# Optimization experiments

Measured on AMD Instinct MI355X. Metric: run time of the kernel, lower is better.

Reference implementation:

```python
import jax, jax.numpy as jnp
import numpy as np

NUM_LETTERS = 33
EMB = 64
HID = 512
KPT = 21
CRD = 3
SEQ = 100
IN0 = EMB * 2 + KPT * CRD * 2  # 254


def setup_inputs() -> dict:
    key = jax.random.key(0)
    ks = jax.random.split(key, 16)
    B = 4096
    s = 0.05
    return {
        "start_letters": jax.random.randint(ks[0], (B,), 0, NUM_LETTERS, dtype=jnp.int32),
        "end_letters": jax.random.randint(ks[1], (B,), 0, NUM_LETTERS, dtype=jnp.int32),
        "start_coords": jax.random.normal(ks[2], (B, KPT * CRD), jnp.float32),
        "end_coords": jax.random.normal(ks[3], (B, KPT * CRD), jnp.float32),
        "emb": jax.random.normal(ks[4], (NUM_LETTERS, EMB), jnp.float32) * s,
        "W_ih0": jax.random.normal(ks[5], (4 * HID, IN0), jnp.float32) * s,
        "W_hh0": jax.random.normal(ks[6], (4 * HID, HID), jnp.float32) * s,
        "b_ih0": jax.random.normal(ks[7], (4 * HID,), jnp.float32) * s,
        "b_hh0": jax.random.normal(ks[8], (4 * HID,), jnp.float32) * s,
        "W_ih1": jax.random.normal(ks[9], (4 * HID, HID), jnp.float32) * s,
        "W_hh1": jax.random.normal(ks[10], (4 * HID, HID), jnp.float32) * s,
        "b_ih1": jax.random.normal(ks[11], (4 * HID,), jnp.float32) * s,
        "b_hh1": jax.random.normal(ks[12], (4 * HID,), jnp.float32) * s,
        "fc_W": jax.random.normal(ks[13], (KPT * CRD, HID), jnp.float32) * s,
        "fc_b": jax.random.normal(ks[14], (KPT * CRD,), jnp.float32) * s,
    }


def _lstm_cell(pre, c):
    # PyTorch gate order: input, forget, cell(g), output
    i, f, g, o = jnp.split(pre, 4, axis=-1)
    c_new = jax.nn.sigmoid(f) * c + jax.nn.sigmoid(i) * jnp.tanh(g)
    h_new = jax.nn.sigmoid(o) * jnp.tanh(c_new)
    return h_new, c_new


def reference(start_letters, end_letters, start_coords, end_coords,
              emb, W_ih0, W_hh0, b_ih0, b_hh0, W_ih1, W_hh1, b_ih1, b_hh1,
              fc_W, fc_b):
    # combined input, constant across timesteps: [B, 254]
    x = jnp.concatenate([emb[start_letters], emb[end_letters],
                         start_coords, end_coords], axis=-1)
    B = x.shape[0]
    # layer-0 input projection is constant per step -> hoist out of the scan
    x0 = x @ W_ih0.T + b_ih0 + b_hh0  # [B, 4H]
    b1 = b_ih1 + b_hh1

    def step(carry, _):
        h0, c0, h1, c1 = carry
        h0, c0 = _lstm_cell(x0 + h0 @ W_hh0.T, c0)
        h1, c1 = _lstm_cell(h0 @ W_ih1.T + b1 + h1 @ W_hh1.T, c1)
        y = h1 @ fc_W.T + fc_b  # [B, 63]
        return (h0, c0, h1, c1), y

    z = jnp.zeros((B, HID), x.dtype)
    _, ys = jax.lax.scan(step, (z, z, z, z), None, length=SEQ)  # [T, B, 63]
    # -> [B, keypoints, coords, T]
    return jnp.moveaxis(ys, 0, -1).reshape(B, KPT, CRD, SEQ)
```

## Files before the change

### kernel.cpp

```cpp
#include <hip/hip_runtime.h>


#define HIDN  512
#define SEQL  100
#define BATCH 4096
#define NB    8
#define BR    128

typedef _Float16 f16;
typedef _Float16 half8 __attribute__((ext_vector_type(8)));
typedef float    f32x4 __attribute__((ext_vector_type(4)));
typedef unsigned int u32x4 __attribute__((ext_vector_type(4)));

#define OFF_XCAT   0ul
#define OFF_X0PT   (OFF_XCAT + 256ul*4096*4)
#define OFF_WP0    (OFF_X0PT + 2048ul*4096*4)
#define OFF_WP1I   (OFF_WP0  + 2048ul*512*2)
#define OFF_WP1H   (OFF_WP1I + 2048ul*512*2)
#define OFF_FCW    (OFF_WP1H + 2048ul*512*2)
#define OFF_B1P    (OFF_FCW  + 64ul*512*2)
#define OFF_H0     (OFF_B1P  + 2048ul*4)
#define OFF_H1     (OFF_H0   + 2ul*4096*512*2)
#define OFF_FLAGS  (OFF_H1   + 2ul*4096*512*2)
#define FLAG_BYTES (32ul*128*4)

__device__ __forceinline__ int orow(int pr){
  return (((pr>>6)&3)<<9) | ((pr>>8)<<6) | (pr&63);
}
__device__ __forceinline__ float sigm(float x){ return 1.f/(1.f + __expf(-x)); }
__device__ __forceinline__ float tanhx(float x){ return 1.f - 2.f/(1.f + __expf(2.f*x)); }
__device__ __forceinline__ f32x4 splat4(float v){ f32x4 r; r[0]=v; r[1]=v; r[2]=v; r[3]=v; return r; }

__global__ __launch_bounds__(256) void k_xcat(
    const int* __restrict__ sl, const int* __restrict__ el,
    const float* __restrict__ sc, const float* __restrict__ ec,
    const float* __restrict__ emb, float* __restrict__ xcatT)
{
  int b = blockIdx.x*256 + threadIdx.x;
  int c = blockIdx.y;
  float v = 0.f;
  if      (c < 64 ) v = emb[sl[b]*64 + c];
  else if (c < 128) v = emb[el[b]*64 + (c-64)];
  else if (c < 191) v = sc[b*63 + (c-128)];
  else if (c < 254) v = ec[b*63 + (c-191)];
  xcatT[c*4096 + b] = v;
}

__global__ __launch_bounds__(256) void k_pack(
    const float* __restrict__ Whh0, const float* __restrict__ Wih1,
    const float* __restrict__ Whh1, const float* __restrict__ fcW,
    const float* __restrict__ bih1, const float* __restrict__ bhh1,
    f16* __restrict__ Wp0, f16* __restrict__ Wp1i, f16* __restrict__ Wp1h,
    f16* __restrict__ fcWp, float* __restrict__ b1p)
{
  int row = blockIdx.x, tid = threadIdx.x;
  if (row < 6144){
    int m  = row >> 11;
    int pr = row & 2047;
    const float* src = (m==0) ? Whh0 : (m==1) ? Wih1 : Whh1;
    f16* dst = (m==0) ? Wp0 : (m==1) ? Wp1i : Wp1h;
    int orig = orow(pr);
    dst[pr*512 + tid      ] = (f16)src[orig*512 + tid      ];
    dst[pr*512 + tid + 256] = (f16)src[orig*512 + tid + 256];
  } else if (row < 6208){
    int n = row - 6144;
    float v0 = (n < 63) ? fcW[n*512 + tid      ] : 0.f;
    float v1 = (n < 63) ? fcW[n*512 + tid + 256] : 0.f;
    fcWp[n*512 + tid] = (f16)v0; fcWp[n*512 + tid + 256] = (f16)v1;
  } else {
    int j = row - 6208;
    int orig = (((tid>>6)&3)<<9) | (j<<6) | (tid&63);
    b1p[j*256 + tid] = bih1[orig] + bhh1[orig];
  }
}

__global__ __launch_bounds__(256) void k_x0(
    const float* __restrict__ xcatT, const float* __restrict__ Wih0,
    const float* __restrict__ bih0, const float* __restrict__ bhh0,
    float* __restrict__ x0pT)
{
  int pr0 = blockIdx.x * 16;
  int b   = blockIdx.y * 256 + threadIdx.x;
  float a[16];
#pragma unroll
  for (int i=0;i<16;i++) a[i] = 0.f;
  for (int k=0;k<254;k++){
    float xv = xcatT[k*4096 + b];
#pragma unroll
    for (int i=0;i<16;i++)
      a[i] = fmaf(xv, Wih0[orow(pr0+i)*254 + k], a[i]);
  }
#pragma unroll
  for (int i=0;i<16;i++){
    int orig = orow(pr0+i);
    x0pT[(size_t)(pr0+i)*4096 + b] = a[i] + bih0[orig] + bhh0[orig];
  }
}

__global__ __launch_bounds__(512, 2) void k_lstm(
    const float* __restrict__ x0pT, const f16* __restrict__ Wp0,
    const f16* __restrict__ Wp1i, const f16* __restrict__ Wp1h,
    const f16* __restrict__ fcWp, const float* __restrict__ b1p,
    const float* __restrict__ fcb, f16* __restrict__ h0buf,
    f16* __restrict__ h1buf, unsigned int* __restrict__ flags,
    float* __restrict__ out)
{
  __shared__ f16 Ach[2][128*40];
  __shared__ f16 Bch[2][256*40];

  const int tid  = threadIdx.x;
  const int blk  = blockIdx.x;
  const int j    = blk & 7;
  const int team = blk >> 3;
  const int b0   = team * BR;
  const int w = tid >> 6, wr = w >> 2, wc = w & 3;
  const int lane = tid & 63, quad = lane >> 4, lc = lane & 15;
  const int ucol = wc*16 + lc;
  const bool des = (j == (team & 7));

  const f16* Wb0  = Wp0  + (size_t)(j*256)*512;
  const f16* Wb1i = Wp1i + (size_t)(j*256)*512;
  const f16* Wb1h = Wp1h + (size_t)(j*256)*512;

  float b1v[4];
#pragma unroll
  for (int g=0; g<4; g++) b1v[g] = b1p[j*256 + g*64 + ucol];
  const float fcbv = (ucol < 63) ? fcb[ucol] : 0.f;

  f32x4 c0[4], c1[4];
#pragma unroll
  for (int mt=0; mt<4; mt++){ c0[mt] = splat4(0.f); c1[mt] = splat4(0.f); }

  const int srA = tid >> 2;
  const int ssg = (tid & 3) * 8;
  unsigned int* tflags = flags + team*128;

  auto barrier = [&](int idx){
    __syncthreads();
    if (tid == 0){
      __threadfence();
      __hip_atomic_fetch_add(&tflags[idx], 1u, __ATOMIC_RELAXED, __HIP_MEMORY_SCOPE_AGENT);
      while (__hip_atomic_load(&tflags[idx], __ATOMIC_RELAXED, __HIP_MEMORY_SCOPE_AGENT) < (unsigned)NB)
        __builtin_amdgcn_s_sleep(4);
      __threadfence();
    }
    __syncthreads();
  };

  auto GEMM = [&](int nch, auto&& Aat, auto&& Bat, f32x4 (&acc)[4][4],
                  bool dofc, f32x4* fca, int fck0){
    u32x4 ra, rb0, rb1;
    auto ld = [&](int kc){
      const f16* Ap = Aat(kc);
      const f16* Bp = Bat(kc);
      ra  = *(const u32x4*)(Ap + (size_t)srA*HIDN + ssg);
      rb0 = *(const u32x4*)(Bp + (size_t)srA*HIDN + ssg);
      rb1 = *(const u32x4*)(Bp + (size_t)(srA+128)*HIDN + ssg);
    };
    auto st = [&](int kc){
      int bu = kc & 1;
      *(u32x4*)&Ach[bu][srA*40 + ssg]        = ra;
      *(u32x4*)&Bch[bu][srA*40 + ssg]        = rb0;
      *(u32x4*)&Bch[bu][(srA+128)*40 + ssg]  = rb1;
    };
    ld(0); st(0);
    if (nch > 1) ld(1);
    for (int kc=0; kc<nch; kc++){
      __syncthreads();
      if (kc+1 < nch){
        st(kc+1);
        if (kc+2 < nch) ld(kc+2);
      }
      const int bu = kc & 1;
      half8 af[4];
#pragma unroll
      for (int mt=0; mt<4; mt++)
        af[mt] = *(const half8*)&Ach[bu][(wr*64 + mt*16 + lc)*40 + quad*8];
#pragma unroll
      for (int g=0; g<4; g++){
        half8 bf = *(const half8*)&Bch[bu][(g*64 + ucol)*40 + quad*8];
#pragma unroll
        for (int mt=0; mt<4; mt++)
          acc[g][mt] = __builtin_amdgcn_mfma_f32_16x16x32_f16(af[mt], bf, acc[g][mt], 0, 0, 0);
      }
      if (dofc && kc >= fck0){
        half8 fb = *(const half8*)(fcWp + (size_t)ucol*HIDN + (kc-fck0)*32 + quad*8);
#pragma unroll
        for (int mt=0; mt<4; mt++)
          fca[mt] = __builtin_amdgcn_mfma_f32_16x16x32_f16(af[mt], fb, fca[mt], 0, 0, 0);
      }
    }
  };

  for (int t=0; t<SEQL; t++){
    const int p  = t & 1;
    const int pp = (t-1) & 1;
    const f16* h0rd = h0buf + (size_t)pp*BATCH*HIDN + (size_t)b0*HIDN;
    const f16* h1rd = h1buf + (size_t)pp*BATCH*HIDN + (size_t)b0*HIDN;
    f16* h0wr = h0buf + (size_t)p*BATCH*HIDN;
    f16* h1wr = h1buf + (size_t)p*BATCH*HIDN;

    f32x4 acc[4][4];
#pragma unroll
    for (int g=0; g<4; g++)
#pragma unroll
      for (int mt=0; mt<4; mt++)
        acc[g][mt] = *(const f32x4*)(x0pT + (size_t)(j*256 + g*64 + ucol)*4096
                                     + b0 + wr*64 + mt*16 + quad*4);
    if (t > 0){
      GEMM(16, [&](int kc){ return h0rd + kc*32; },
               [&](int kc){ return Wb0  + kc*32; },
           acc, false, (f32x4*)nullptr, 0);
    }
#pragma unroll
    for (int mt=0; mt<4; mt++){
#pragma unroll
      for (int r=0; r<4; r++){
        float iv = sigm(acc[0][mt][r]);
        float fv = sigm(acc[1][mt][r]);
        float gv = tanhx(acc[2][mt][r]);
        float ov = sigm(acc[3][mt][r]);
        float cn = fv*c0[mt][r] + iv*gv;
        c0[mt][r] = cn;
        float hn = ov * tanhx(cn);
        int row = wr*64 + mt*16 + quad*4 + r;
        h0wr[(size_t)(b0+row)*HIDN + j*64 + ucol] = (f16)hn;
      }
    }
    barrier(t);

    const f16* h0cur = h0buf + (size_t)p*BATCH*HIDN + (size_t)b0*HIDN;
#pragma unroll
    for (int g=0; g<4; g++)
#pragma unroll
      for (int mt=0; mt<4; mt++)
        acc[g][mt] = splat4(b1v[g]);
    f32x4 fca[4];
#pragma unroll
    for (int mt=0; mt<4; mt++) fca[mt] = splat4(fcbv);

    if (t > 0){
      GEMM(32, [&](int kc){ return kc < 16 ? h0cur + kc*32 : h1rd  + (kc-16)*32; },
               [&](int kc){ return kc < 16 ? Wb1i  + kc*32 : Wb1h + (kc-16)*32; },
           acc, des, fca, 16);
      if (des && ucol < 63){
#pragma unroll
        for (int mt=0; mt<4; mt++)
#pragma unroll
          for (int r=0; r<4; r++){
            int row = wr*64 + mt*16 + quad*4 + r;
            out[((b0+row)*63 + ucol)*100 + (t-1)] = fca[mt][r];
          }
      }
    } else {
      GEMM(16, [&](int kc){ return h0cur + kc*32; },
               [&](int kc){ return Wb1i  + kc*32; },
           acc, false, (f32x4*)nullptr, 0);
    }
#pragma unroll
    for (int mt=0; mt<4; mt++){
#pragma unroll
      for (int r=0; r<4; r++){
        float iv = sigm(acc[0][mt][r]);
        float fv = sigm(acc[1][mt][r]);
        float gv = tanhx(acc[2][mt][r]);
        float ov = sigm(acc[3][mt][r]);
        float cn = fv*c1[mt][r] + iv*gv;
        c1[mt][r] = cn;
        float hn = ov * tanhx(cn);
        int row = wr*64 + mt*16 + quad*4 + r;
        h1wr[(size_t)(b0+row)*HIDN + j*64 + ucol] = (f16)hn;
      }
    }
  }

  barrier(SEQL);
  if (des){
    const f16* h1last = h1buf + (size_t)1*BATCH*HIDN + (size_t)b0*HIDN;
    f32x4 fca[4];
#pragma unroll
    for (int mt=0; mt<4; mt++) fca[mt] = splat4(fcbv);
    for (int kc=0; kc<16; kc++){
      __syncthreads();
      *(u32x4*)&Ach[0][srA*40 + ssg] = *(const u32x4*)(h1last + (size_t)srA*HIDN + kc*32 + ssg);
      __syncthreads();
      half8 af[4];
#pragma unroll
      for (int mt=0; mt<4; mt++)
        af[mt] = *(const half8*)&Ach[0][(wr*64 + mt*16 + lc)*40 + quad*8];
      half8 fb = *(const half8*)(fcWp + (size_t)ucol*HIDN + kc*32 + quad*8);
#pragma unroll
      for (int mt=0; mt<4; mt++)
        fca[mt] = __builtin_amdgcn_mfma_f32_16x16x32_f16(af[mt], fb, fca[mt], 0, 0, 0);
    }
    if (ucol < 63){
#pragma unroll
      for (int mt=0; mt<4; mt++)
#pragma unroll
        for (int r=0; r<4; r++){
          int row = wr*64 + mt*16 + quad*4 + r;
          out[((b0+row)*63 + ucol)*100 + 99] = fca[mt][r];
        }
    }
  }
}

extern "C" void kernel_launch(void* const* d_in, const int* in_sizes, int n_in,
                              void* d_out, int out_size, void* d_ws, size_t ws_size,
                              hipStream_t stream)
{
  const int*   sl   = (const int*)  d_in[0];
  const int*   el   = (const int*)  d_in[1];
  const float* sc   = (const float*)d_in[2];
  const float* ec   = (const float*)d_in[3];
  const float* emb  = (const float*)d_in[4];
  const float* Wih0 = (const float*)d_in[5];
  const float* Whh0 = (const float*)d_in[6];
  const float* bih0 = (const float*)d_in[7];
  const float* bhh0 = (const float*)d_in[8];
  const float* Wih1 = (const float*)d_in[9];
  const float* Whh1 = (const float*)d_in[10];
  const float* bih1 = (const float*)d_in[11];
  const float* bhh1 = (const float*)d_in[12];
  const float* fcW  = (const float*)d_in[13];
  const float* fcb  = (const float*)d_in[14];

  char* ws = (char*)d_ws;
  float* xcatT = (float*)(ws + OFF_XCAT);
  float* x0pT  = (float*)(ws + OFF_X0PT);
  f16*   Wp0   = (f16*)  (ws + OFF_WP0);
  f16*   Wp1i  = (f16*)  (ws + OFF_WP1I);
  f16*   Wp1h  = (f16*)  (ws + OFF_WP1H);
  f16*   fcWp  = (f16*)  (ws + OFF_FCW);
  float* b1p   = (float*)(ws + OFF_B1P);
  f16*   h0b   = (f16*)  (ws + OFF_H0);
  f16*   h1b   = (f16*)  (ws + OFF_H1);
  unsigned int* flags = (unsigned int*)(ws + OFF_FLAGS);

  hipMemsetAsync(flags, 0, FLAG_BYTES, stream);
  k_xcat<<<dim3(16, 256), 256, 0, stream>>>(sl, el, sc, ec, emb, xcatT);
  k_pack<<<6216, 256, 0, stream>>>(Whh0, Wih1, Whh1, fcW, bih1, bhh1,
                                   Wp0, Wp1i, Wp1h, fcWp, b1p);
  k_x0<<<dim3(128, 16), 256, 0, stream>>>(xcatT, Wih0, bih0, bhh0, x0pT);
  k_lstm<<<256, 512, 0, stream>>>(x0pT, Wp0, Wp1i, Wp1h, fcWp, b1p, fcb,
                                  h0b, h1b, flags, (float*)d_out);
}
```

Measured before the change: 8.291 ms.

## Pre-swizzle weights into MFMA fragment layout and stage larger swizzled A tiles

Weights are repacked on the device into per-lane MFMA fragment order, so each lane loads its B fragments directly from global memory with software prefetch two k-chunks ahead, and B no longer goes through LDS. The A (hidden state) tile is staged in halves of 256 columns into a single XOR-swizzled LDS buffer, which cuts the number of __syncthreads per GEMM from one per k-chunk to a few per pass. The x0 projection is also written in a fragment-friendly layout so accumulator initialisation becomes contiguous vector loads. The trade-off is more registers per thread and a larger LDS footprint (64KB), which may limit occupancy at two blocks per CU.

After: 17.84 ms. 2.15x slower.

```diff
diff --git a/kernel.cpp b/kernel.cpp
--- a/kernel.cpp
+++ b/kernel.cpp
@@ -13,12 +13,12 @@
 typedef unsigned int u32x4 __attribute__((ext_vector_type(4)));
 
 #define OFF_XCAT   0ul
-#define OFF_X0PT   (OFF_XCAT + 256ul*4096*4)
-#define OFF_WP0    (OFF_X0PT + 2048ul*4096*4)
-#define OFF_WP1I   (OFF_WP0  + 2048ul*512*2)
-#define OFF_WP1H   (OFF_WP1I + 2048ul*512*2)
-#define OFF_FCW    (OFF_WP1H + 2048ul*512*2)
-#define OFF_B1P    (OFF_FCW  + 64ul*512*2)
+#define OFF_X0F    (OFF_XCAT + 256ul*4096*4)
+#define OFF_BF0    (OFF_X0F  + 2048ul*4096*4)
+#define OFF_BF1I   (OFF_BF0  + 2048ul*512*2)
+#define OFF_BF1H   (OFF_BF1I + 2048ul*512*2)
+#define OFF_FCF    (OFF_BF1H + 2048ul*512*2)
+#define OFF_B1P    (OFF_FCF  + 64ul*512*2)
 #define OFF_H0     (OFF_B1P  + 2048ul*4)
 #define OFF_H1     (OFF_H0   + 2ul*4096*512*2)
 #define OFF_FLAGS  (OFF_H1   + 2ul*4096*512*2)
@@ -50,34 +50,55 @@
     const float* __restrict__ Whh0, const float* __restrict__ Wih1,
     const float* __restrict__ Whh1, const float* __restrict__ fcW,
     const float* __restrict__ bih1, const float* __restrict__ bhh1,
-    f16* __restrict__ Wp0, f16* __restrict__ Wp1i, f16* __restrict__ Wp1h,
-    f16* __restrict__ fcWp, float* __restrict__ b1p)
+    f16* __restrict__ BF0, f16* __restrict__ BF1i, f16* __restrict__ BF1h,
+    f16* __restrict__ fcF, float* __restrict__ b1p)
 {
-  int row = blockIdx.x, tid = threadIdx.x;
-  if (row < 6144){
-    int m  = row >> 11;
-    int pr = row & 2047;
+  int bx = blockIdx.x, t = threadIdx.x;
+  if (bx < 384){
+    int m   = bx / 128;
+    int rem = bx % 128;
+    int jj = rem >> 4, g = (rem >> 2) & 3, wc = rem & 3;
     const float* src = (m==0) ? Whh0 : (m==1) ? Wih1 : Whh1;
-    f16* dst = (m==0) ? Wp0 : (m==1) ? Wp1i : Wp1h;
-    int orig = orow(pr);
-    dst[pr*512 + tid      ] = (f16)src[orig*512 + tid      ];
-    dst[pr*512 + tid + 256] = (f16)src[orig*512 + tid + 256];
-  } else if (row < 6208){
-    int n = row - 6144;
-    float v0 = (n < 63) ? fcW[n*512 + tid      ] : 0.f;
-    float v1 = (n < 63) ? fcW[n*512 + tid + 256] : 0.f;
-    fcWp[n*512 + tid] = (f16)v0; fcWp[n*512 + tid + 256] = (f16)v1;
+    f16* dst = (m==0) ? BF0 : (m==1) ? BF1i : BF1h;
+    size_t fb = (size_t)(((jj*4+g)*4+wc)*16) * 512;
+    for (int s=0; s<4; s++){
+      int pid = t + s*256;
+      int kc = pid >> 6, lane = pid & 63;
+      int lcc = lane & 15, qd = lane >> 4;
+      int orig = g*512 + jj*64 + wc*16 + lcc;
+      const float* sp = src + (size_t)orig*512 + kc*32 + qd*8;
+      f16* d = dst + fb + (size_t)kc*512 + lane*8;
+#pragma unroll
+      for (int e=0; e<8; e++) d[e] = (f16)sp[e];
+    }
+  } else if (bx < 388){
+    int wc = bx - 384;
+    for (int s=0; s<4; s++){
+      int pid = t + s*256;
+      int kc = pid >> 6, lane = pid & 63;
+      int lcc = lane & 15, qd = lane >> 4;
+      int col = wc*16 + lcc;
+      f16* d = fcF + (size_t)(wc*16 + kc)*512 + lane*8;
+      if (col < 63){
+        const float* sp = fcW + (size_t)col*512 + kc*32 + qd*8;
+#pragma unroll
+        for (int e=0; e<8; e++) d[e] = (f16)sp[e];
+      } else {
+#pragma unroll
+        for (int e=0; e<8; e++) d[e] = (f16)0.f;
+      }
+    }
   } else {
-    int j = row - 6208;
-    int orig = (((tid>>6)&3)<<9) | (j<<6) | (tid&63);
-    b1p[j*256 + tid] = bih1[orig] + bhh1[orig];
+    int jj = bx - 388;
+    int orig = (((t>>6)&3)<<9) | (jj<<6) | (t&63);
+    b1p[jj*256 + t] = bih1[orig] + bhh1[orig];
   }
 }
 
 __global__ __launch_bounds__(256) void k_x0(
     const float* __restrict__ xcatT, const float* __restrict__ Wih0,
     const float* __restrict__ bih0, const float* __restrict__ bhh0,
-    float* __restrict__ x0pT)
+    float* __restrict__ x0F)
 {
   int pr0 = blockIdx.x * 16;
   int b   = blockIdx.y * 256 + threadIdx.x;
@@ -90,23 +111,27 @@
     for (int i=0;i<16;i++)
       a[i] = fmaf(xv, Wih0[orow(pr0+i)*254 + k], a[i]);
   }
+  int team = b>>7, wrr = (b>>6)&1, mtt = (b>>4)&3, qd = (b>>2)&3, r = b&3;
 #pragma unroll
   for (int i=0;i<16;i++){
-    int orig = orow(pr0+i);
-    x0pT[(size_t)(pr0+i)*4096 + b] = a[i] + bih0[orig] + bhh0[orig];
+    int pr = pr0 + i;
+    int orig = orow(pr);
+    int jj = pr>>8, g = (pr>>6)&3, u = pr&63, wcc = u>>4, lcc = u&15;
+    size_t idx = (size_t)team*262144 + (size_t)jj*32768 + g*8192 + wrr*4096
+               + mtt*1024 + wcc*256 + (qd*16 + lcc)*4 + r;
+    x0F[idx] = a[i] + bih0[orig] + bhh0[orig];
   }
 }
 
 __global__ __launch_bounds__(512, 2) void k_lstm(
-    const float* __restrict__ x0pT, const f16* __restrict__ Wp0,
-    const f16* __restrict__ Wp1i, const f16* __restrict__ Wp1h,
-    const f16* __restrict__ fcWp, const float* __restrict__ b1p,
+    const float* __restrict__ x0F, const f16* __restrict__ BF0,
+    const f16* __restrict__ BF1i, const f16* __restrict__ BF1h,
+    const f16* __restrict__ fcF, const float* __restrict__ b1p,
     const float* __restrict__ fcb, f16* __restrict__ h0buf,
     f16* __restrict__ h1buf, unsigned int* __restrict__ flags,
     float* __restrict__ out)
 {
-  __shared__ f16 Ach[2][128*40];
-  __shared__ f16 Bch[2][256*40];
+  __shared__ f16 Ash[128*256];
 
   const int tid  = threadIdx.x;
   const int blk  = blockIdx.x;
@@ -118,9 +143,13 @@
   const int ucol = wc*16 + lc;
   const bool des = (j == (team & 7));
 
-  const f16* Wb0  = Wp0  + (size_t)(j*256)*512;
-  const f16* Wb1i = Wp1i + (size_t)(j*256)*512;
-  const f16* Wb1h = Wp1h + (size_t)(j*256)*512;
+  const size_t fboff = (size_t)(((j*4)*4+wc)*16)*512 + lane*8;
+  const f16* Bb0  = BF0  + fboff;
+  const f16* Bb1i = BF1i + fboff;
+  const f16* Bb1h = BF1h + fboff;
+  const f16* fcp = fcF + (size_t)(wc*16)*512 + lane*8;
+  const float* x0p = x0F + (size_t)team*262144 + (size_t)j*32768
+                   + wr*4096 + wc*256 + lane*4;
 
   float b1v[4];
 #pragma unroll
@@ -131,10 +160,13 @@
 #pragma unroll
   for (int mt=0; mt<4; mt++){ c0[mt] = splat4(0.f); c1[mt] = splat4(0.f); }
 
-  const int srA = tid >> 2;
-  const int ssg = (tid & 3) * 8;
+  const int srow  = tid >> 2;
+  const int sslot = tid & 3;
+  const int swzb  = (quad*16) ^ ((lc&3)<<4);
+  const int swzf  = (lc&4)<<4;
+  char* Abase = (char*)Ash + (wr*64 + lc)*512 + swzb;
+
   unsigned int* tflags = flags + team*128;
-
   auto barrier = [&](int idx){
     __syncthreads();
     if (tid == 0){
@@ -147,56 +179,86 @@
     __syncthreads();
   };
 
-  auto GEMM = [&](int nch, auto&& Aat, auto&& Bat, f32x4 (&acc)[4][4],
-                  bool dofc, f32x4* fca, int fck0){
-    u32x4 ra, rb0, rb1;
-    auto ld = [&](int kc){
-      const f16* Ap = Aat(kc);
-      const f16* Bp = Bat(kc);
-      ra  = *(const u32x4*)(Ap + (size_t)srA*HIDN + ssg);
-      rb0 = *(const u32x4*)(Bp + (size_t)srA*HIDN + ssg);
-      rb1 = *(const u32x4*)(Bp + (size_t)(srA+128)*HIDN + ssg);
-    };
-    auto st = [&](int kc){
-      int bu = kc & 1;
-      *(u32x4*)&Ach[bu][srA*40 + ssg]        = ra;
-      *(u32x4*)&Bch[bu][srA*40 + ssg]        = rb0;
-      *(u32x4*)&Bch[bu][(srA+128)*40 + ssg]  = rb1;
-    };
-    ld(0); st(0);
-    if (nch > 1) ld(1);
-    for (int kc=0; kc<nch; kc++){
+  auto LD8 = [&](const f16* src, u32x4 (&v)[8]){
+#pragma unroll
+    for (int i=0;i<8;i++)
+      v[i] = *(const u32x4*)(src + (size_t)srow*HIDN + (sslot + i*4)*8);
+  };
+  auto ST8 = [&](const u32x4 (&v)[8]){
+#pragma unroll
+    for (int i=0;i<8;i++){
+      int cb = ((sslot + i*4)*16) ^ ((srow&7)<<4);
+      *(u32x4*)((char*)Ash + srow*512 + cb) = v[i];
+    }
+  };
+
+  auto PASS = [&](const f16* src, const f16* Bb, bool dofc,
+                  f32x4 (&acc)[4][4], f32x4* fca){
+    half8 bcur[4], bnxt[4], fcur{}, fnxt{};
+#pragma unroll
+    for (int g=0; g<4; g++){
+      bcur[g] = *(const half8*)(Bb + (size_t)g*32768);
+      bnxt[g] = *(const half8*)(Bb + (size_t)g*32768 + 512);
+    }
+    if (dofc){ fcur = *(const half8*)(fcp); fnxt = *(const half8*)(fcp + 512); }
+    u32x4 sv[8];
+    LD8(src, sv);
+#pragma unroll
+    for (int kh=0; kh<2; kh++){
+      ST8(sv);
       __syncthreads();
-      if (kc+1 < nch){
-        st(kc+1);
-        if (kc+2 < nch) ld(kc+2);
-      }
-      const int bu = kc & 1;
-      half8 af[4];
+      if (kh == 0) LD8(src + 256, sv);
+      half8 aC[4];
 #pragma unroll
       for (int mt=0; mt<4; mt++)
-        af[mt] = *(const half8*)&Ach[bu][(wr*64 + mt*16 + lc)*40 + quad*8];
-#pragma unroll
-      for (int g=0; g<4; g++){
-        half8 bf = *(const half8*)&Bch[bu][(g*64 + ucol)*40 + quad*8];
-#pragma unroll
-        for (int mt=0; mt<4; mt++)
-          acc[g][mt] = __builtin_amdgcn_mfma_f32_16x16x32_f16(af[mt], bf, acc[g][mt], 0, 0, 0);
-      }
-      if (dofc && kc >= fck0){
-        half8 fb = *(const half8*)(fcWp + (size_t)ucol*HIDN + (kc-fck0)*32 + quad*8);
-#pragma unroll
-        for (int mt=0; mt<4; mt++)
-          fca[mt] = __builtin_amdgcn_mfma_f32_16x16x32_f16(af[mt], fb, fca[mt], 0, 0, 0);
-      }
+        aC[mt] = *(const half8*)(Abase + mt*8192 + swzf);
+#pragma unroll
+      for (int kq=0; kq<8; kq++){
+        const int kc = kh*8 + kq;
+        half8 aN[4];
+        if (kq < 7){
+          const int colx = ((kq+1)*64) ^ swzf;
+#pragma unroll
+          for (int mt=0; mt<4; mt++)
+            aN[mt] = *(const half8*)(Abase + mt*8192 + colx);
+        }
+        half8 bpre[4], fpre{};
+        const bool havepre = (kc + 2 < 16);
+        if (havepre){
+#pragma unroll
+          for (int g=0; g<4; g++)
+            bpre[g] = *(const half8*)(Bb + (size_t)g*32768 + (kc+2)*512);
+          if (dofc) fpre = *(const half8*)(fcp + (kc+2)*512);
+        }
+#pragma unroll
+        for (int g=0; g<4; g++)
+#pragma unroll
+          for (int mt=0; mt<4; mt++)
+            acc[g][mt] = __builtin_amdgcn_mfma_f32_16x16x32_f16(aC[mt], bcur[g], acc[g][mt], 0, 0, 0);
+        if (dofc)
+#pragma unroll
+          for (int mt=0; mt<4; mt++)
+            fca[mt] = __builtin_amdgcn_mfma_f32_16x16x32_f16(aC[mt], fcur, fca[mt], 0, 0, 0);
+#pragma unroll
+        for (int g=0; g<4; g++) bcur[g] = bnxt[g];
+        if (dofc) fcur = fnxt;
+        if (havepre){
+#pragma unroll
+          for (int g=0; g<4; g++) bnxt[g] = bpre[g];
+          if (dofc) fnxt = fpre;
+        }
+        if (kq < 7){
+#pragma unroll
+          for (int mt=0; mt<4; mt++) aC[mt] = aN[mt];
+        }
+      }
+      __syncthreads();
     }
   };
 
   for (int t=0; t<SEQL; t++){
     const int p  = t & 1;
     const int pp = (t-1) & 1;
-    const f16* h0rd = h0buf + (size_t)pp*BATCH*HIDN + (size_t)b0*HIDN;
-    const f16* h1rd = h1buf + (size_t)pp*BATCH*HIDN + (size_t)b0*HIDN;
     f16* h0wr = h0buf + (size_t)p*BATCH*HIDN;
     f16* h1wr = h1buf + (size_t)p*BATCH*HIDN;
 
@@ -205,12 +267,9 @@
     for (int g=0; g<4; g++)
 #pragma unroll
       for (int mt=0; mt<4; mt++)
-        acc[g][mt] = *(const f32x4*)(x0pT + (size_t)(j*256 + g*64 + ucol)*4096
-                                     + b0 + wr*64 + mt*16 + quad*4);
+        acc[g][mt] = *(const f32x4*)(x0p + g*8192 + mt*1024);
     if (t > 0){
-      GEMM(16, [&](int kc){ return h0rd + kc*32; },
-               [&](int kc){ return Wb0  + kc*32; },
-           acc, false, (f32x4*)nullptr, 0);
+      PASS(h0buf + (size_t)pp*BATCH*HIDN + (size_t)b0*HIDN, Bb0, false, acc, nullptr);
     }
 #pragma unroll
     for (int mt=0; mt<4; mt++){
@@ -229,7 +288,6 @@
     }
     barrier(t);
 
-    const f16* h0cur = h0buf + (size_t)p*BATCH*HIDN + (size_t)b0*HIDN;
 #pragma unroll
     for (int g=0; g<4; g++)
 #pragma unroll
@@ -239,10 +297,9 @@
 #pragma unroll
     for (int mt=0; mt<4; mt++) fca[mt] = splat4(fcbv);
 
+    PASS(h0buf + (size_t)p*BATCH*HIDN + (size_t)b0*HIDN, Bb1i, false, acc, nullptr);
     if (t > 0){
-      GEMM(32, [&](int kc){ return kc < 16 ? h0cur + kc*32 : h1rd  + (kc-16)*32; },
-               [&](int kc){ return kc < 16 ? Wb1i  + kc*32 : Wb1h + (kc-16)*32; },
-           acc, des, fca, 16);
+      PASS(h1buf + (size_t)pp*BATCH*HIDN + (size_t)b0*HIDN, Bb1h, des, acc, fca);
       if (des && ucol < 63){
 #pragma unroll
         for (int mt=0; mt<4; mt++)
@@ -252,10 +309,6 @@
             out[((b0+row)*63 + ucol)*100 + (t-1)] = fca[mt][r];
           }
       }
-    } else {
-      GEMM(16, [&](int kc){ return h0cur + kc*32; },
-               [&](int kc){ return Wb1i  + kc*32; },
-           acc, false, (f32x4*)nullptr, 0);
     }
 #pragma unroll
     for (int mt=0; mt<4; mt++){
@@ -280,18 +333,26 @@
     f32x4 fca[4];
 #pragma unroll
     for (int mt=0; mt<4; mt++) fca[mt] = splat4(fcbv);
-    for (int kc=0; kc<16; kc++){
+    u32x4 sv[8];
+#pragma unroll
+    for (int kh=0; kh<2; kh++){
+      LD8(h1last + kh*256, sv);
+      ST8(sv);
       __syncthreads();
-      *(u32x4*)&Ach[0][srA*40 + ssg] = *(const u32x4*)(h1last + (size_t)srA*HIDN + kc*32 + ssg);
+#pragma unroll
+      for (int kq=0; kq<8; kq++){
+        int kc = kh*8 + kq;
+        half8 af[4];
+        const int colx = (kq*64) ^ swzf;
+#pragma unroll
+        for (int mt=0; mt<4; mt++)
+          af[mt] = *(const half8*)(Abase + mt*8192 + colx);
+        half8 fb = *(const half8*)(fcp + (size_t)kc*512);
+#pragma unroll
+        for (int mt=0; mt<4; mt++)
+          fca[mt] = __builtin_amdgcn_mfma_f32_16x16x32_f16(af[mt], fb, fca[mt], 0, 0, 0);
+      }
       __syncthreads();
-      half8 af[4];
-#pragma unroll
-      for (int mt=0; mt<4; mt++)
-        af[mt] = *(const half8*)&Ach[0][(wr*64 + mt*16 + lc)*40 + quad*8];
-      half8 fb = *(const half8*)(fcWp + (size_t)ucol*HIDN + kc*32 + quad*8);
-#pragma unroll
-      for (int mt=0; mt<4; mt++)
-        fca[mt] = __builtin_amdgcn_mfma_f32_16x16x32_f16(af[mt], fb, fca[mt], 0, 0, 0);
     }
     if (ucol < 63){
 #pragma unroll
@@ -327,11 +388,11 @@
 
   char* ws = (char*)d_ws;
   float* xcatT = (float*)(ws + OFF_XCAT);
-  float* x0pT  = (float*)(ws + OFF_X0PT);
-  f16*   Wp0   = (f16*)  (ws + OFF_WP0);
-  f16*   Wp1i  = (f16*)  (ws + OFF_WP1I);
-  f16*   Wp1h  = (f16*)  (ws + OFF_WP1H);
-  f16*   fcWp  = (f16*)  (ws + OFF_FCW);
+  float* x0F   = (float*)(ws + OFF_X0F);
+  f16*   BF0   = (f16*)  (ws + OFF_BF0);
+  f16*   BF1i  = (f16*)  (ws + OFF_BF1I);
+  f16*   BF1h  = (f16*)  (ws + OFF_BF1H);
+  f16*   fcF   = (f16*)  (ws + OFF_FCF);
   float* b1p   = (float*)(ws + OFF_B1P);
   f16*   h0b   = (f16*)  (ws + OFF_H0);
   f16*   h1b   = (f16*)  (ws + OFF_H1);
@@ -339,9 +400,9 @@
 
   hipMemsetAsync(flags, 0, FLAG_BYTES, stream);
   k_xcat<<<dim3(16, 256), 256, 0, stream>>>(sl, el, sc, ec, emb, xcatT);
-  k_pack<<<6216, 256, 0, stream>>>(Whh0, Wih1, Whh1, fcW, bih1, bhh1,
-                                   Wp0, Wp1i, Wp1h, fcWp, b1p);
-  k_x0<<<dim3(128, 16), 256, 0, stream>>>(xcatT, Wih0, bih0, bhh0, x0pT);
-  k_lstm<<<256, 512, 0, stream>>>(x0pT, Wp0, Wp1i, Wp1h, fcWp, b1p, fcb,
+  k_pack<<<396, 256, 0, stream>>>(Whh0, Wih1, Whh1, fcW, bih1, bhh1,
+                                  BF0, BF1i, BF1h, fcF, b1p);
+  k_x0<<<dim3(128, 16), 256, 0, stream>>>(xcatT, Wih0, bih0, bhh0, x0F);
+  k_lstm<<<256, 512, 0, stream>>>(x0F, BF0, BF1i, BF1h, fcF, b1p, fcb,
                                   h0b, h1b, flags, (float*)d_out);
 }
```
